# Optimization experiments

Measured on AMD Instinct MI355X. Metric: run time of the kernel, lower is better.

## Reference

```python
import jax, jax.numpy as jnp
import numpy as np

B, S, E = 4, 4096, 512

def setup_inputs() -> dict:
    key = jax.random.key(0)
    ks = jax.random.split(key, 9)
    scale = 1.0 / np.sqrt(E)  # keep linear weights at realistic init scale
    return {
        "query": jax.random.normal(ks[0], (B, S, E), jnp.float32),
        "key":   jax.random.normal(ks[1], (B, S, E), jnp.float32),
        "value": jax.random.normal(ks[2], (B, S, E), jnp.float32),
        "Wq": jax.random.normal(ks[3], (E, E), jnp.float32) * scale,
        "bq": jax.random.normal(ks[4], (E,), jnp.float32) * scale,
        "Wk": jax.random.normal(ks[5], (E, E), jnp.float32) * scale,
        "bk": jax.random.normal(ks[6], (E,), jnp.float32) * scale,
        "Wv": jax.random.normal(ks[7], (E, E), jnp.float32) * scale,
        "bv": jax.random.normal(ks[8], (E,), jnp.float32) * scale,
    }

def reference(query, key, value, Wq, bq, Wk, bk, Wv, bv):
    # torch Linear: x @ W^T + b
    q = jnp.einsum('bse,oe->bso', query, Wq) + bq
    k = jnp.einsum('bse,oe->bso', key,   Wk) + bk
    v = jnp.einsum('bse,oe->bso', value, Wv) + bv
    # NOTE: module applies NO 1/sqrt(d) scaling (faithful to source)
    scores = jnp.einsum('bqd,bkd->bqk', q, k)          # [B,S,S] materialized
    attn = jax.nn.softmax(scores, axis=-1)
    # dropout is identity in eval / for deterministic reference
    return jnp.einsum('bqk,bkd->bqd', attn, v)         # [B,S,E]
```

## Files before the change

kernel.cpp:

```cpp
#include <hip/hip_runtime.h>

typedef __attribute__((ext_vector_type(8))) _Float16 f16x8;
typedef __attribute__((ext_vector_type(4))) _Float16 f16x4;
typedef __attribute__((ext_vector_type(4))) float f32x4;

#define NB 4
#define NS 4096
#define NE 512

__device__ __forceinline__ f16x8 cvt2(float4 a, float4 b) {
    f16x8 r;
    r[0] = (_Float16)a.x; r[1] = (_Float16)a.y; r[2] = (_Float16)a.z; r[3] = (_Float16)a.w;
    r[4] = (_Float16)b.x; r[5] = (_Float16)b.y; r[6] = (_Float16)b.z; r[7] = (_Float16)b.w;
    return r;
}
__device__ __forceinline__ void gload_lds16(const void* g, void* l) {
    __builtin_amdgcn_global_load_lds(
        (const __attribute__((address_space(1))) void*)g,
        (__attribute__((address_space(3))) void*)l, 16, 0, 0);
}

template <int CTRL>
__device__ __forceinline__ float dpp_ror(float x) {
    int r = __builtin_amdgcn_update_dpp(
        0, __builtin_bit_cast(int, x), CTRL, 0xF, 0xF, true);
    return __builtin_bit_cast(float, r);
}
__device__ __forceinline__ float rmax16(float x) {
    x = fmaxf(x, dpp_ror<0x128>(x));
    x = fmaxf(x, dpp_ror<0x124>(x));
    x = fmaxf(x, dpp_ror<0x122>(x));
    x = fmaxf(x, dpp_ror<0x121>(x));
    return x;
}
__device__ __forceinline__ float rsum16(float x) {
    x += dpp_ror<0x128>(x);
    x += dpp_ror<0x124>(x);
    x += dpp_ror<0x122>(x);
    x += dpp_ror<0x121>(x);
    return x;
}

__global__ __launch_bounds__(256, 2) void proj_kernel(
    const float* __restrict__ Xq, const float* __restrict__ Xk,
    const float* __restrict__ Xv,
    const float* __restrict__ Wq, const float* __restrict__ Wk,
    const float* __restrict__ Wv,
    const float* __restrict__ bq, const float* __restrict__ bk,
    const float* __restrict__ bv,
    _Float16* __restrict__ oq, _Float16* __restrict__ ok,
    _Float16* __restrict__ ovt, int b0)
{
    __shared__ __align__(16) _Float16 As[2][128 * 32];
    __shared__ __align__(16) _Float16 Bs[2][128 * 32];
    const int t = threadIdx.x;
    const int w = t >> 6, ln = t & 63;
    const int which = blockIdx.y;
    const float* X    = (which == 0) ? Xq : ((which == 1) ? Xk : Xv);
    const float* W    = (which == 0) ? Wq : ((which == 1) ? Wk : Wv);
    const float* bias = (which == 0) ? bq : ((which == 1) ? bk : bv);

    const int m0 = (blockIdx.x >> 2) * 128;
    const int n0 = (blockIdx.x & 3) * 128;

    const int srow  = t >> 1;
    const int shalf = (t & 1) * 16;
    const float* gA = X + ((size_t)b0 * NS + m0 + srow) * NE + shalf;
    const float* gB = W + (size_t)(n0 + srow) * NE + shalf;

    f32x4 acc[4][4] = {};
    const int wm = (w >> 1) * 64, wn = (w & 1) * 64;
    const int lcol = ln & 15, lq = ln >> 4;

    float4 ra[4], rb[4], na[4], nb[4];

    auto LOAD = [&](int k0, float4* da, float4* db) {
        da[0] = *(const float4*)(gA + k0);
        da[1] = *(const float4*)(gA + k0 + 4);
        da[2] = *(const float4*)(gA + k0 + 8);
        da[3] = *(const float4*)(gA + k0 + 12);
        db[0] = *(const float4*)(gB + k0);
        db[1] = *(const float4*)(gB + k0 + 4);
        db[2] = *(const float4*)(gB + k0 + 8);
        db[3] = *(const float4*)(gB + k0 + 12);
    };
    auto WRITE = [&](int p, const float4* da, const float4* db) {
        *(f16x8*)&As[p][srow * 32 + shalf]     = cvt2(da[0], da[1]);
        *(f16x8*)&As[p][srow * 32 + shalf + 8] = cvt2(da[2], da[3]);
        *(f16x8*)&Bs[p][srow * 32 + shalf]     = cvt2(db[0], db[1]);
        *(f16x8*)&Bs[p][srow * 32 + shalf + 8] = cvt2(db[2], db[3]);
    };
    auto COMPUTE = [&](int p) {
        f16x8 a[4], b[4];
#pragma unroll
        for (int i = 0; i < 4; i++)
            a[i] = *(const f16x8*)&As[p][(wm + i * 16 + lcol) * 32 + lq * 8];
#pragma unroll
        for (int j = 0; j < 4; j++)
            b[j] = *(const f16x8*)&Bs[p][(wn + j * 16 + lcol) * 32 + lq * 8];
#pragma unroll
        for (int i = 0; i < 4; i++)
#pragma unroll
            for (int j = 0; j < 4; j++)
                acc[i][j] = __builtin_amdgcn_mfma_f32_16x16x32_f16(a[i], b[j], acc[i][j], 0, 0, 0);
    };

    LOAD(0, ra, rb);
    asm volatile("s_waitcnt vmcnt(0)" ::: "memory");
    WRITE(0, ra, rb);
    LOAD(32, na, nb);
    asm volatile("s_waitcnt lgkmcnt(0)" ::: "memory");
    __builtin_amdgcn_s_barrier();
    asm volatile("" ::: "memory");

#pragma unroll
    for (int kk = 0; kk < 8; kk++) {
        COMPUTE(0);
        asm volatile("s_waitcnt vmcnt(0)" ::: "memory");
        WRITE(1, na, nb);
        if (2 * kk + 2 < 16) LOAD((2 * kk + 2) * 32, ra, rb);
        asm volatile("s_waitcnt lgkmcnt(0)" ::: "memory");
        __builtin_amdgcn_s_barrier();
        asm volatile("" ::: "memory");
        COMPUTE(1);
        if (2 * kk + 2 < 16) {
            asm volatile("s_waitcnt vmcnt(0)" ::: "memory");
            WRITE(0, ra, rb);
            if (2 * kk + 3 < 16) LOAD((2 * kk + 3) * 32, na, nb);
            asm volatile("s_waitcnt lgkmcnt(0)" ::: "memory");
            __builtin_amdgcn_s_barrier();
            asm volatile("" ::: "memory");
        }
    }

    if (which == 0) {
#pragma unroll
        for (int j = 0; j < 4; j++) {
            const int col = n0 + wn + j * 16 + lcol;
            const float bb = bias[col];
#pragma unroll
            for (int i = 0; i < 4; i++) {
                const int rbase = m0 + wm + i * 16 + lq * 4;
#pragma unroll
                for (int r = 0; r < 4; r++)
                    oq[(size_t)(rbase + r) * NE + col] = (_Float16)(acc[i][j][r] + bb);
            }
        }
    } else if (which == 1) {
#pragma unroll
        for (int j = 0; j < 4; j++) {
            const int col = n0 + wn + j * 16 + lcol;
            const int cch = col >> 3, clo = col & 7;
            const float bb = bias[col];
#pragma unroll
            for (int i = 0; i < 4; i++) {
                const int rbase = m0 + wm + i * 16 + lq * 4;
#pragma unroll
                for (int r = 0; r < 4; r++) {
                    const int s = rbase + r;
                    ok[(size_t)s * NE + ((cch ^ (s & 7)) << 3) + clo] =
                        (_Float16)(acc[i][j][r] + bb);
                }
            }
        }
    } else {
#pragma unroll
        for (int j = 0; j < 4; j++) {
            const int d = n0 + wn + j * 16 + lcol;
            const float bb = bias[d];
#pragma unroll
            for (int i = 0; i < 4; i++) {
                const int rbase = m0 + wm + i * 16 + lq * 4;
                const int bat = rbase >> 12;
                const int sl  = rbase & 4095;
                const int kc  = sl >> 6;
                const int slot = ((sl >> 3) & 7) ^ (d & 7);
                f16x4 pk;
#pragma unroll
                for (int r = 0; r < 4; r++) pk[r] = (_Float16)(acc[i][j][r] + bb);
                *(f16x4*)&ovt[(((size_t)bat * 64 + kc) * NE + d) * 64 + slot * 8 + (sl & 7)] = pk;
            }
        }
    }
}

__global__ __launch_bounds__(512, 2) void attn_kernel(
    const _Float16* __restrict__ q, const _Float16* __restrict__ ksw,
    const _Float16* __restrict__ vsw, float* __restrict__ out, int b0)
{
    __shared__ __align__(16) _Float16 Kb[64 * 512];
    __shared__ __align__(16) _Float16 Vb[512 * 64];
    __shared__ __align__(16) _Float16 Pb[64 * 72];
    __shared__ float mpart[2][64];
    __shared__ float lpart[2][64];

    const int t = threadIdx.x, w = t >> 6, ln = t & 63;
    const int lcol = ln & 15, lq = ln >> 4;
    const int rt = w & 3, g = w >> 2;
    const int xm = lcol & 7;

    int qx, rel;
    if (gridDim.y == 4) {
        const int id = blockIdx.x + (blockIdx.y << 6);
        const int xcd = id & 7, slot = id >> 3;
        rel = xcd >> 1;
        qx  = ((xcd & 1) << 5) + slot;
    } else { qx = blockIdx.x; rel = blockIdx.y; }
    const int babs = b0 + rel;
    const int q0 = qx * 64;

    const _Float16* qp = q + ((size_t)rel * NS + q0 + rt * 16 + lcol) * NE + lq * 8;
    f16x8 qf[16];
#pragma unroll
    for (int ks = 0; ks < 16; ks++) qf[ks] = *(const f16x8*)(qp + ks * 32);

    const _Float16* kbase = ksw + (size_t)rel * NS * NE;
    const _Float16* vbase = vsw + (size_t)rel * NS * NE;

    auto stageK = [&](int kc) {
        const _Float16* src = kbase + (size_t)kc * 64 * NE;
#pragma unroll
        for (int i = 0; i < 8; i++) {
            const int blk = i * 8 + w;
            gload_lds16(src + (size_t)blk * 512 + ln * 8, (_Float16*)Kb + blk * 512);
        }
    };
    auto stageV = [&](int kc) {
        const _Float16* src = vbase + (size_t)kc * NE * 64;
#pragma unroll
        for (int i = 0; i < 8; i++) {
            const int blk = i * 8 + w;
            gload_lds16(src + (size_t)blk * 512 + ln * 8, (_Float16*)Vb + blk * 512);
        }
    };

    f32x4 oacc[16] = {};
    float m_st[4] = {-1e30f, -1e30f, -1e30f, -1e30f};
    float l_st[4] = {0.f, 0.f, 0.f, 0.f};

    asm volatile("" ::: "memory");
    stageK(0);
    stageV(0);

    for (int kc = 0; kc < 64; kc++) {
        asm volatile("s_waitcnt vmcnt(8)" ::: "memory");
        __builtin_amdgcn_s_barrier();
        asm volatile("" ::: "memory");

        f32x4 s0 = {}, s1 = {};
        __builtin_amdgcn_s_setprio(1);
#pragma unroll
        for (int ks = 0; ks < 16; ks++) {
            const int ch = ((ks * 4 + lq) ^ xm) * 8;
            f16x8 kb0 = *(const f16x8*)&Kb[(g * 32 + lcol) * 512 + ch];
            f16x8 kb1 = *(const f16x8*)&Kb[(g * 32 + 16 + lcol) * 512 + ch];
            s0 = __builtin_amdgcn_mfma_f32_16x16x32_f16(qf[ks], kb0, s0, 0, 0, 0);
            s1 = __builtin_amdgcn_mfma_f32_16x16x32_f16(qf[ks], kb1, s1, 0, 0, 0);
        }
        __builtin_amdgcn_s_setprio(0);

        asm volatile("" ::: "memory");
        __builtin_amdgcn_s_barrier();
        asm volatile("" ::: "memory");
        if (kc < 63) stageK(kc + 1);

        float Mg[4];
#pragma unroll
        for (int r = 0; r < 4; r++) {
            float mx = rmax16(fmaxf(s0[r], s1[r]));
            Mg[r] = fmaxf(m_st[r], mx);
            const float p0 = __expf(s0[r] - Mg[r]);
            const float p1 = __expf(s1[r] - Mg[r]);
            const int row = rt * 16 + lq * 4 + r;
            Pb[row * 72 + g * 32 + lcol]      = (_Float16)p0;
            Pb[row * 72 + g * 32 + 16 + lcol] = (_Float16)p1;
            const float ls = rsum16(p0 + p1);
            if (lcol == 0) { mpart[g][row] = Mg[r]; lpart[g][row] = ls; }
        }

        if (kc < 63) { asm volatile("s_waitcnt vmcnt(8) lgkmcnt(0)" ::: "memory"); }
        else         { asm volatile("s_waitcnt vmcnt(0) lgkmcnt(0)" ::: "memory"); }
        __builtin_amdgcn_s_barrier();
        asm volatile("" ::: "memory");

        float alpha[4];
#pragma unroll
        for (int r = 0; r < 4; r++) {
            const int row = rt * 16 + lq * 4 + r;
            const float M0 = mpart[0][row], M1 = mpart[1][row];
            const float mn = fmaxf(M0, M1);
            alpha[r] = __expf(m_st[r] - mn);
            l_st[r] = l_st[r] * alpha[r]
                    + __expf(M0 - mn) * lpart[0][row]
                    + __expf(M1 - mn) * lpart[1][row];
            m_st[r] = mn;
        }
        const bool allone = (alpha[0] == 1.f) & (alpha[1] == 1.f) &
                            (alpha[2] == 1.f) & (alpha[3] == 1.f);
        if (!__all(allone)) {
#pragma unroll
            for (int et = 0; et < 16; et++) {
                oacc[et][0] *= alpha[0]; oacc[et][1] *= alpha[1];
                oacc[et][2] *= alpha[2]; oacc[et][3] *= alpha[3];
            }
        }

        const int frow = rt * 16 + lcol;
        const float F0 = mpart[0][frow], F1 = mpart[1][frow];
        const float fm = fmaxf(F0, F1);
        const _Float16 c0 = (_Float16)__expf(F0 - fm);
        const _Float16 c1 = (_Float16)__expf(F1 - fm);
        f16x8 pa0 = *(const f16x8*)&Pb[frow * 72 + lq * 8];
        f16x8 pa1 = *(const f16x8*)&Pb[frow * 72 + 32 + lq * 8];
#pragma unroll
        for (int j = 0; j < 8; j++) { pa0[j] *= c0; pa1[j] *= c1; }

        __builtin_amdgcn_s_setprio(1);
#pragma unroll
        for (int et = 0; et < 16; et++) {
            const int e = g * 256 + et * 16 + lcol;
            f16x8 v0 = *(const f16x8*)&Vb[e * 64 + ((lq ^ xm) * 8)];
            f16x8 v1 = *(const f16x8*)&Vb[e * 64 + (((4 + lq) ^ xm) * 8)];
            oacc[et] = __builtin_amdgcn_mfma_f32_16x16x32_f16(pa0, v0, oacc[et], 0, 0, 0);
            oacc[et] = __builtin_amdgcn_mfma_f32_16x16x32_f16(pa1, v1, oacc[et], 0, 0, 0);
        }
        __builtin_amdgcn_s_setprio(0);

        asm volatile("" ::: "memory");
        __builtin_amdgcn_s_barrier();
        asm volatile("" ::: "memory");
        if (kc < 63) stageV(kc + 1);
    }

#pragma unroll
    for (int r = 0; r < 4; r++) {
        const float inv = 1.0f / l_st[r];
        const size_t ob = ((size_t)babs * NS + q0 + rt * 16 + lq * 4 + r) * NE + g * 256 + lcol;
#pragma unroll
        for (int et = 0; et < 16; et++)
            out[ob + et * 16] = oacc[et][r] * inv;
    }
}

extern "C" void kernel_launch(void* const* d_in, const int* in_sizes, int n_in,
                              void* d_out, int out_size, void* d_ws, size_t ws_size,
                              hipStream_t stream) {
    const float* query = (const float*)d_in[0];
    const float* key_  = (const float*)d_in[1];
    const float* value = (const float*)d_in[2];
    const float* Wq    = (const float*)d_in[3];
    const float* bq    = (const float*)d_in[4];
    const float* Wk    = (const float*)d_in[5];
    const float* bk    = (const float*)d_in[6];
    const float* Wv    = (const float*)d_in[7];
    const float* bv    = (const float*)d_in[8];

    const size_t per_batch = (size_t)3 * NS * NE * 2;
    int nb_chunk = (int)(ws_size / per_batch);
    if (nb_chunk > NB) nb_chunk = NB;
    if (nb_chunk < 1)  nb_chunk = 1;

    _Float16* qh  = (_Float16*)d_ws;
    _Float16* kh  = qh + (size_t)nb_chunk * NS * NE;
    _Float16* vth = kh + (size_t)nb_chunk * NS * NE;

    for (int b0 = 0; b0 < NB; b0 += nb_chunk) {
        int nb = NB - b0 < nb_chunk ? NB - b0 : nb_chunk;
        proj_kernel<<<dim3(nb * 128, 3, 1), 256, 0, stream>>>(
            query, key_, value, Wq, Wk, Wv, bq, bk, bv, qh, kh, vth, b0);
        attn_kernel<<<dim3(NS / 64, nb, 1), 512, 0, stream>>>(
            qh, kh, vth, (float*)d_out, b0);
    }
}
```

Measured before the change: 445.6 us.

## Repartition PV stage so each wave covers all query rows over a 64-column slice

The P·V output tiling changes. Before, each wave owned one 16-row query tile and 256 output columns (16 V fragments). Now each wave owns all four 16-row query tiles and a 64-column slice (w*64), so every V fragment loaded from LDS is reused across four MFMAs instead of one. The intent is to cut LDS traffic for V. In exchange, every wave must track softmax max/sum state for all 64 rows and load and rescale four P fragments. It also adds m_home tracking so the QK stage still uses the running max of its own row tile.

After: 1.052 ms. 2.36x slower.

```diff
diff --git a/kernel.cpp b/kernel.cpp
--- a/kernel.cpp
+++ b/kernel.cpp
@@ -234,9 +234,13 @@
         }
     };
 
-    f32x4 oacc[16] = {};
-    float m_st[4] = {-1e30f, -1e30f, -1e30f, -1e30f};
-    float l_st[4] = {0.f, 0.f, 0.f, 0.f};
+    f32x4 oacc[4][4] = {};
+    float m_st[4][4], l_st[4][4];
+#pragma unroll
+    for (int qt = 0; qt < 4; qt++)
+#pragma unroll
+        for (int r = 0; r < 4; r++) { m_st[qt][r] = -1e30f; l_st[qt][r] = 0.f; }
+    float m_home[4] = {-1e30f, -1e30f, -1e30f, -1e30f};
 
     asm volatile("" ::: "memory");
     stageK(0);
@@ -264,18 +268,17 @@
         asm volatile("" ::: "memory");
         if (kc < 63) stageK(kc + 1);
 
-        float Mg[4];
 #pragma unroll
         for (int r = 0; r < 4; r++) {
             float mx = rmax16(fmaxf(s0[r], s1[r]));
-            Mg[r] = fmaxf(m_st[r], mx);
-            const float p0 = __expf(s0[r] - Mg[r]);
-            const float p1 = __expf(s1[r] - Mg[r]);
+            const float mg = fmaxf(m_home[r], mx);
+            const float p0 = __expf(s0[r] - mg);
+            const float p1 = __expf(s1[r] - mg);
             const int row = rt * 16 + lq * 4 + r;
             Pb[row * 72 + g * 32 + lcol]      = (_Float16)p0;
             Pb[row * 72 + g * 32 + 16 + lcol] = (_Float16)p1;
             const float ls = rsum16(p0 + p1);
-            if (lcol == 0) { mpart[g][row] = Mg[r]; lpart[g][row] = ls; }
+            if (lcol == 0) { mpart[g][row] = mg; lpart[g][row] = ls; }
         }
 
         if (kc < 63) { asm volatile("s_waitcnt vmcnt(8) lgkmcnt(0)" ::: "memory"); }
@@ -283,46 +286,62 @@
         __builtin_amdgcn_s_barrier();
         asm volatile("" ::: "memory");
 
-        float alpha[4];
-#pragma unroll
-        for (int r = 0; r < 4; r++) {
-            const int row = rt * 16 + lq * 4 + r;
-            const float M0 = mpart[0][row], M1 = mpart[1][row];
-            const float mn = fmaxf(M0, M1);
-            alpha[r] = __expf(m_st[r] - mn);
-            l_st[r] = l_st[r] * alpha[r]
-                    + __expf(M0 - mn) * lpart[0][row]
-                    + __expf(M1 - mn) * lpart[1][row];
-            m_st[r] = mn;
-        }
-        const bool allone = (alpha[0] == 1.f) & (alpha[1] == 1.f) &
-                            (alpha[2] == 1.f) & (alpha[3] == 1.f);
+        float alpha[4][4];
+        bool allone = true;
+#pragma unroll
+        for (int qt = 0; qt < 4; qt++) {
+#pragma unroll
+            for (int r = 0; r < 4; r++) {
+                const int row = qt * 16 + lq * 4 + r;
+                const float M0 = mpart[0][row], M1 = mpart[1][row];
+                const float mn = fmaxf(M0, M1);
+                const float a = __expf(m_st[qt][r] - mn);
+                l_st[qt][r] = l_st[qt][r] * a
+                            + __expf(M0 - mn) * lpart[0][row]
+                            + __expf(M1 - mn) * lpart[1][row];
+                m_st[qt][r] = mn;
+                if (qt == rt) m_home[r] = mn;
+                alpha[qt][r] = a;
+                allone = allone & (a == 1.f);
+            }
+        }
         if (!__all(allone)) {
 #pragma unroll
-            for (int et = 0; et < 16; et++) {
-                oacc[et][0] *= alpha[0]; oacc[et][1] *= alpha[1];
-                oacc[et][2] *= alpha[2]; oacc[et][3] *= alpha[3];
-            }
-        }
-
-        const int frow = rt * 16 + lcol;
-        const float F0 = mpart[0][frow], F1 = mpart[1][frow];
-        const float fm = fmaxf(F0, F1);
-        const _Float16 c0 = (_Float16)__expf(F0 - fm);
-        const _Float16 c1 = (_Float16)__expf(F1 - fm);
-        f16x8 pa0 = *(const f16x8*)&Pb[frow * 72 + lq * 8];
-        f16x8 pa1 = *(const f16x8*)&Pb[frow * 72 + 32 + lq * 8];
-#pragma unroll
-        for (int j = 0; j < 8; j++) { pa0[j] *= c0; pa1[j] *= c1; }
+            for (int qt = 0; qt < 4; qt++)
+#pragma unroll
+                for (int et = 0; et < 4; et++) {
+                    oacc[qt][et][0] *= alpha[qt][0];
+                    oacc[qt][et][1] *= alpha[qt][1];
+                    oacc[qt][et][2] *= alpha[qt][2];
+                    oacc[qt][et][3] *= alpha[qt][3];
+                }
+        }
+
+        f16x8 pa0[4], pa1[4];
+#pragma unroll
+        for (int qt = 0; qt < 4; qt++) {
+            const int frow = qt * 16 + lcol;
+            const float F0 = mpart[0][frow], F1 = mpart[1][frow];
+            const float fm = fmaxf(F0, F1);
+            const _Float16 c0 = (_Float16)__expf(F0 - fm);
+            const _Float16 c1 = (_Float16)__expf(F1 - fm);
+            pa0[qt] = *(const f16x8*)&Pb[frow * 72 + lq * 8];
+            pa1[qt] = *(const f16x8*)&Pb[frow * 72 + 32 + lq * 8];
+#pragma unroll
+            for (int j = 0; j < 8; j++) { pa0[qt][j] *= c0; pa1[qt][j] *= c1; }
+        }
 
         __builtin_amdgcn_s_setprio(1);
 #pragma unroll
-        for (int et = 0; et < 16; et++) {
-            const int e = g * 256 + et * 16 + lcol;
+        for (int et = 0; et < 4; et++) {
+            const int e = w * 64 + et * 16 + lcol;
             f16x8 v0 = *(const f16x8*)&Vb[e * 64 + ((lq ^ xm) * 8)];
             f16x8 v1 = *(const f16x8*)&Vb[e * 64 + (((4 + lq) ^ xm) * 8)];
-            oacc[et] = __builtin_amdgcn_mfma_f32_16x16x32_f16(pa0, v0, oacc[et], 0, 0, 0);
-            oacc[et] = __builtin_amdgcn_mfma_f32_16x16x32_f16(pa1, v1, oacc[et], 0, 0, 0);
+#pragma unroll
+            for (int qt = 0; qt < 4; qt++) {
+                oacc[qt][et] = __builtin_amdgcn_mfma_f32_16x16x32_f16(pa0[qt], v0, oacc[qt][et], 0, 0, 0);
+                oacc[qt][et] = __builtin_amdgcn_mfma_f32_16x16x32_f16(pa1[qt], v1, oacc[qt][et], 0, 0, 0);
+            }
         }
         __builtin_amdgcn_s_setprio(0);
 
@@ -333,13 +352,16 @@
     }
 
 #pragma unroll
-    for (int r = 0; r < 4; r++) {
-        const float inv = 1.0f / l_st[r];
-        const size_t ob = ((size_t)babs * NS + q0 + rt * 16 + lq * 4 + r) * NE + g * 256 + lcol;
-#pragma unroll
-        for (int et = 0; et < 16; et++)
-            out[ob + et * 16] = oacc[et][r] * inv;
-    }
+    for (int qt = 0; qt < 4; qt++)
+#pragma unroll
+        for (int r = 0; r < 4; r++) {
+            const float inv = 1.0f / l_st[qt][r];
+            const size_t ob = ((size_t)babs * NS + q0 + qt * 16 + lq * 4 + r) * NE
+                            + w * 64 + lcol;
+#pragma unroll
+            for (int et = 0; et < 4; et++)
+                out[ob + et * 16] = oacc[qt][et][r] * inv;
+        }
 }
 
 extern "C" void kernel_launch(void* const* d_in, const int* in_sizes, int n_in,
```
